# Kernel optimization log

Hardware: AMD Instinct MI355X
Metric: run time of the kernel (lower is better)

The kernel has to match this reference:

```python
import jax, jax.numpy as jnp
import numpy as np

B, C, L = 64, 21, 1024
D_MODEL, PATCH_LEN, STRIDE = 768, 16, 8


def setup_inputs() -> dict:
    key = jax.random.key(0)
    k1, k2, k3, k4 = jax.random.split(key, 4)
    x = jax.random.normal(k1, (B, C, L), dtype=jnp.float32)
    # Conv1d(patch_len -> d_model, k=3, circular, no bias), kaiming-ish scale
    conv_w = jax.random.normal(k2, (D_MODEL, PATCH_LEN, 3), dtype=jnp.float32) * (2.0 / (PATCH_LEN * 3)) ** 0.5
    w1 = jax.random.normal(k3, (D_MODEL, D_MODEL), dtype=jnp.float32) / np.float32(np.sqrt(D_MODEL))
    b1 = jnp.zeros((D_MODEL,), dtype=jnp.float32)
    w2 = jax.random.normal(k4, (D_MODEL, D_MODEL), dtype=jnp.float32) / np.float32(np.sqrt(D_MODEL))
    b2 = jnp.zeros((D_MODEL,), dtype=jnp.float32)
    return {"x": x, "conv_w": conv_w, "w1": w1, "b1": b1, "w2": w2, "b2": b2, "reverse": 0}


def _patchify(x):
    # ReplicationPad1d((0, stride)) then unfold(size=patch_len, step=stride)
    xp = jnp.pad(x, ((0, 0), (0, 0), (0, STRIDE)), mode="edge")  # (B,C,L+stride)
    P = (xp.shape[-1] - PATCH_LEN) // STRIDE + 1
    idx = jnp.arange(P)[:, None] * STRIDE + jnp.arange(PATCH_LEN)[None, :]  # (P, patch_len)
    patches = xp[:, :, idx]  # (B, C, P, patch_len)
    return patches.reshape(x.shape[0] * x.shape[1], P, PATCH_LEN)


def _token_embed(blocks, conv_w):
    # Conv1d over the patch axis, circular padding=1, no bias.
    h = blocks.transpose(0, 2, 1)  # (BN, patch_len, P)
    hp = jnp.concatenate([h[:, :, -1:], h, h[:, :, :1]], axis=-1)  # circular pad 1
    out = jax.lax.conv_general_dilated(
        hp, conv_w, window_strides=(1,), padding="VALID",
        dimension_numbers=("NCH", "OIH", "NCH"))  # (BN, d_model, P)
    return out.transpose(0, 2, 1)  # (BN, P, d_model)


def reference(x, conv_w, w1, b1, w2, b2, reverse):
    blocks = _patchify(x)  # (B*C, P, patch_len)
    # Note: in the original torch code, the reverse/cluster-flip branch writes
    # into a temporary produced by boolean indexing -> it is a value no-op.
    # reverse=0 here, so blocks pass through unchanged (faithful).
    emb = _token_embed(blocks, conv_w)  # (BN, P, d_model)
    pos = jnp.maximum(emb @ w1 + b1, 0.0) @ w2 + b2  # Linear-ReLU-Linear position MLP
    out = emb + pos  # dropout is identity at eval / p=0
    return out
```

## Files before the change

kernel.cpp:

```cpp
#include <hip/hip_runtime.h>
#include <hip/hip_bf16.h>

typedef __bf16 bf16x8 __attribute__((ext_vector_type(8)));
typedef float floatx4 __attribute__((ext_vector_type(4)));
typedef unsigned short ushort_t;
typedef ushort_t ushort8 __attribute__((ext_vector_type(8)));

#define KD 768

__global__ __launch_bounds__(256) void transpose_cvt_kernel(
    const float* __restrict__ src, __hip_bfloat16* __restrict__ dst) {
  __shared__ float tile[32][33];
  const int bx = blockIdx.x % 24;
  const int by = blockIdx.x / 24;
  const int tx = threadIdx.x & 31;
  const int ty = threadIdx.x >> 5;
#pragma unroll
  for (int i = 0; i < 32; i += 8)
    tile[ty + i][tx] = src[(size_t)(by * 32 + ty + i) * KD + bx * 32 + tx];
  __syncthreads();
#pragma unroll
  for (int i = 0; i < 32; i += 8)
    dst[(size_t)(bx * 32 + ty + i) * KD + by * 32 + tx] =
        __float2bfloat16(tile[tx][ty + i]);
}

__global__ __launch_bounds__(256) void w1c_kernel(
    const float* __restrict__ cw, const float* __restrict__ w1,
    __hip_bfloat16* __restrict__ w1ct) {
  __shared__ float wcrow[768];
  const int e = blockIdx.x;
  const int nb = blockIdx.y * 256 + threadIdx.x;
  const int i = e & 15, kk = e >> 4;
  for (int o = threadIdx.x; o < 768; o += 256)
    wcrow[o] = cw[(size_t)o * 48 + i * 3 + kk];
  __syncthreads();
  float acc = 0.f;
  for (int o = 0; o < 768; ++o)
    acc = fmaf(wcrow[o], w1[(size_t)o * KD + nb], acc);
  w1ct[(size_t)nb * 64 + e] = __float2bfloat16(acc);
  if (e == 0) {
#pragma unroll
    for (int ez = 48; ez < 64; ++ez)
      w1ct[(size_t)nb * 64 + ez] = __float2bfloat16(0.f);
  }
}

__global__ __launch_bounds__(128) void patchify_kernel(
    const float* __restrict__ x, __hip_bfloat16* __restrict__ P) {
  __shared__ float xs[1032];
  const int n = blockIdx.x;
  const int tid = threadIdx.x;
  const float* xr = x + (size_t)n * 1024;
  const float4* xr4 = (const float4*)xr;
  float4* xs4 = (float4*)xs;
  for (int j = tid; j < 256; j += 128) xs4[j] = xr4[j];
  if (tid < 8) xs[1024 + tid] = xr[1023];
  __syncthreads();
  const int p = tid;
  __hip_bfloat16 row[64];
#pragma unroll
  for (int kk = 0; kk < 3; ++kk) {
    const int q = (p + kk + 127) & 127;
#pragma unroll
    for (int i = 0; i < 16; ++i)
      row[kk * 16 + i] = __float2bfloat16(xs[q * 8 + i]);
  }
#pragma unroll
  for (int i = 48; i < 64; ++i) row[i] = __float2bfloat16(0.f);
  __hip_bfloat16* pr = P + ((size_t)n * 128 + p) * 64;
#pragma unroll
  for (int s = 0; s < 8; ++s)
    *(ushort8*)&pr[s * 8] = *(const ushort8*)&row[s * 8];
}

__device__ __forceinline__ void load_patch(const float* __restrict__ xr,
                                           int qw, float* b) {
  if (qw < 127) {
    const float4* p4 = (const float4*)(xr + qw * 8);
    float4 v0 = p4[0], v1 = p4[1], v2 = p4[2], v3 = p4[3];
    b[0] = v0.x; b[1] = v0.y; b[2] = v0.z; b[3] = v0.w;
    b[4] = v1.x; b[5] = v1.y; b[6] = v1.z; b[7] = v1.w;
    b[8] = v2.x; b[9] = v2.y; b[10] = v2.z; b[11] = v2.w;
    b[12] = v3.x; b[13] = v3.y; b[14] = v3.z; b[15] = v3.w;
  } else {
    float4 v0 = *(const float4*)(xr + 1016);
    float4 v1 = *(const float4*)(xr + 1020);
    b[0] = v0.x; b[1] = v0.y; b[2] = v0.z; b[3] = v0.w;
    b[4] = v1.x; b[5] = v1.y; b[6] = v1.z; b[7] = v1.w;
    float e = v1.w;
#pragma unroll
    for (int i = 8; i < 16; ++i) b[i] = e;
  }
}

__global__ __launch_bounds__(256) void conv_kernel(
    const float* __restrict__ x, const float* __restrict__ cw,
    __hip_bfloat16* __restrict__ emb, int nb) {
  const int lb = blockIdx.x;
  const int n = nb + lb;
  const float* xr = x + (size_t)n * 1024;
  const int o = blockIdx.y * 256 + threadIdx.x;

  float w[48];
  const float4* wp = (const float4*)(cw + (size_t)o * 48);
#pragma unroll
  for (int q = 0; q < 12; ++q) {
    float4 v = wp[q];
    w[q * 4 + 0] = v.x; w[q * 4 + 1] = v.y;
    w[q * 4 + 2] = v.z; w[q * 4 + 3] = v.w;
  }

  __hip_bfloat16* erow = emb + (size_t)lb * 128 * KD + o;
  float P0[16], P1[16], P2[16], P3[16];

  auto pair = [&](const float* Pa, const float* Pb, const float* Pc,
                  const float* Pd, int p) {
    float a0 = 0.f, a1 = 0.f;
#pragma unroll
    for (int i = 0; i < 16; ++i) {
      a0 += w[i * 3 + 0] * Pa[i];
      a0 += w[i * 3 + 1] * Pb[i];
      a0 += w[i * 3 + 2] * Pc[i];
      a1 += w[i * 3 + 0] * Pb[i];
      a1 += w[i * 3 + 1] * Pc[i];
      a1 += w[i * 3 + 2] * Pd[i];
    }
    erow[(size_t)p * KD] = __float2bfloat16(a0);
    erow[(size_t)(p + 1) * KD] = __float2bfloat16(a1);
  };

  load_patch(xr, 127, P0);
  load_patch(xr, 0, P1);
  for (int p = 0; p < 128; p += 4) {
    load_patch(xr, p + 1, P2);
    load_patch(xr, (p + 2) & 127, P3);
    pair(P0, P1, P2, P3, p);
    load_patch(xr, (p + 3) & 127, P0);
    load_patch(xr, (p + 4) & 127, P1);
    pair(P2, P3, P0, P1, p + 2);
  }
}

__global__ __launch_bounds__(512, 2) void pgemm_kernel(
    const __hip_bfloat16* __restrict__ P, const __hip_bfloat16* __restrict__ Bt,
    const float* __restrict__ bias, __hip_bfloat16* __restrict__ out) {
  __shared__ __align__(16) ushort_t As[256 * 64];
  __shared__ __align__(16) ushort_t Bs[256 * 64];
  const int tid = threadIdx.x;
  const int lane = tid & 63;
  const int w = __builtin_amdgcn_readfirstlane(tid >> 6);
  const int m0 = blockIdx.x * 256;
  const int n0 = blockIdx.y * 256;

  const int srow = tid >> 3;
  const int schunk = (tid & 7) ^ (srow & 7);
  const size_t ga = (size_t)(m0 + srow) * 64 + schunk * 8;
  const size_t gb = (size_t)(n0 + srow) * 64 + schunk * 8;
  typedef __attribute__((address_space(3))) void lv_t;
  typedef __attribute__((address_space(1))) const void gv_t;
  const int dw = w * 1024;
#pragma unroll
  for (int i = 0; i < 4; ++i)
    __builtin_amdgcn_global_load_lds(
        (gv_t*)(P + ga + (size_t)(i * 64) * 64),
        (lv_t*)((char*)&As[0] + i * 8192 + dw), 16, 0, 0);
#pragma unroll
  for (int i = 0; i < 4; ++i)
    __builtin_amdgcn_global_load_lds(
        (gv_t*)(Bt + gb + (size_t)(i * 64) * 64),
        (lv_t*)((char*)&Bs[0] + i * 8192 + dw), 16, 0, 0);
  asm volatile("s_waitcnt vmcnt(0)\n\ts_barrier" ::: "memory");

  const int rl = lane & 15;
  const int ql = lane >> 4;
  const int wm = (w >> 2) * 128;
  const int wn = (w & 3) * 64;
  const int so0 = (ql ^ (rl & 7)) * 8;
  const int ra = (wm + rl) * 64;
  const int rb = (wn + rl) * 64;

  floatx4 acc[8][4];
#pragma unroll
  for (int mi = 0; mi < 8; ++mi)
#pragma unroll
    for (int nj = 0; nj < 4; ++nj) acc[mi][nj] = (floatx4){0.f, 0.f, 0.f, 0.f};

#pragma unroll
  for (int ks = 0; ks < 2; ++ks) {
    const int so = so0 ^ (ks * 32);
    bf16x8 av[8], bv[4];
#pragma unroll
    for (int mi = 0; mi < 8; ++mi)
      av[mi] =
          __builtin_bit_cast(bf16x8, *(const ushort8*)&As[ra + mi * 1024 + so]);
#pragma unroll
    for (int nj = 0; nj < 4; ++nj)
      bv[nj] =
          __builtin_bit_cast(bf16x8, *(const ushort8*)&Bs[rb + nj * 1024 + so]);
#pragma unroll
    for (int mi = 0; mi < 8; ++mi)
#pragma unroll
      for (int nj = 0; nj < 4; ++nj)
        acc[mi][nj] = __builtin_amdgcn_mfma_f32_16x16x32_bf16(
            av[mi], bv[nj], acc[mi][nj], 0, 0, 0);
  }

#pragma unroll
  for (int nj = 0; nj < 4; ++nj) {
    const int cc = n0 + wn + nj * 16 + rl;
    const float bvs = bias[cc];
#pragma unroll
    for (int mi = 0; mi < 8; ++mi) {
      const int rbase = m0 + wm + mi * 16 + ql * 4;
#pragma unroll
      for (int p = 0; p < 4; ++p) {
        float v = acc[mi][nj][p] + bvs;
        v = v > 0.f ? v : 0.f;
        out[(size_t)(rbase + p) * KD + cc] = __float2bfloat16(v);
      }
    }
  }
}

template <int MODE>
__global__ __launch_bounds__(512, 2) void gemm_kernel(
    const __hip_bfloat16* __restrict__ A, const __hip_bfloat16* __restrict__ Bt,
    const float* __restrict__ bias, const __hip_bfloat16* __restrict__ emb,
    void* __restrict__ outp, int mt) {
  __shared__ __align__(16) ushort_t As[3 * 256 * 64];
  __shared__ __align__(16) ushort_t Bs[3 * 128 * 64];
  const int tid = threadIdx.x;
  const int lane = tid & 63;
  const int w = __builtin_amdgcn_readfirstlane(tid >> 6);

  const int total = mt * 6;
  const int q8 = total >> 3, r8 = total & 7;
  const int xcd = blockIdx.x & 7;
  const int j8 = blockIdx.x >> 3;
  const int wg =
      (xcd < r8 ? xcd * (q8 + 1) : r8 * (q8 + 1) + (xcd - r8) * q8) + j8;
  const int m0 = (wg / 6) * 256;
  const int n0 = (wg % 6) * 128;

  const int srow = tid >> 3;
  const int schunk = (tid & 7) ^ (srow & 7);
  const size_t ga = (size_t)(m0 + srow) * KD + schunk * 8;
  const size_t gb = (size_t)(n0 + srow) * KD + schunk * 8;
  typedef __attribute__((address_space(3))) void lv_t;
  typedef __attribute__((address_space(1))) const void gv_t;
  const int dw = w * 1024;

  auto stageA = [&](int t, int r3, int i) {
    __builtin_amdgcn_global_load_lds(
        (gv_t*)(A + ga + (size_t)(i * 64) * KD + t * 64),
        (lv_t*)((char*)&As[0] + r3 * 32768 + i * 8192 + dw), 16, 0, 0);
  };
  auto stageB = [&](int t, int r3, int j) {
    __builtin_amdgcn_global_load_lds(
        (gv_t*)(Bt + gb + (size_t)(j * 64) * KD + t * 64),
        (lv_t*)((char*)&Bs[0] + r3 * 16384 + j * 8192 + dw), 16, 0, 0);
  };

  const int rl = lane & 15;
  const int ql = lane >> 4;
  const int wm = (w >> 1) * 64;
  const int wn = (w & 1) * 64;
  const int so0 = (ql ^ (rl & 7)) * 8;
  const int ra = (wm + rl) * 64;
  const int rb = (wn + rl) * 64;

  floatx4 acc[4][4];
#pragma unroll
  for (int mi = 0; mi < 4; ++mi)
#pragma unroll
    for (int nj = 0; nj < 4; ++nj) acc[mi][nj] = (floatx4){0.f, 0.f, 0.f, 0.f};

#pragma unroll
  for (int i = 0; i < 4; ++i) stageA(0, 0, i);
#pragma unroll
  for (int j = 0; j < 2; ++j) stageB(0, 0, j);
#pragma unroll
  for (int i = 0; i < 4; ++i) stageA(1, 1, i);
#pragma unroll
  for (int j = 0; j < 2; ++j) stageB(1, 1, j);
  asm volatile("s_waitcnt vmcnt(6)\n\ts_barrier" ::: "memory");

  int rc = 0, rs = 2;
  for (int t = 0; t < 12; ++t) {
    const ushort_t* Ab = &As[rc * 16384];
    const ushort_t* Bb = &Bs[rc * 8192];
    bf16x8 av[4], bv[4];

#pragma unroll
    for (int mi = 0; mi < 4; ++mi)
      av[mi] =
          __builtin_bit_cast(bf16x8, *(const ushort8*)&Ab[ra + mi * 1024 + so0]);
#pragma unroll
    for (int nj = 0; nj < 4; ++nj)
      bv[nj] =
          __builtin_bit_cast(bf16x8, *(const ushort8*)&Bb[rb + nj * 1024 + so0]);
    if (t < 10) {
      stageA(t + 2, rs, 0);
      stageA(t + 2, rs, 1);
      stageA(t + 2, rs, 2);
    }
    asm volatile("s_barrier" ::: "memory");
    __builtin_amdgcn_s_setprio(1);
#pragma unroll
    for (int mi = 0; mi < 4; ++mi)
#pragma unroll
      for (int nj = 0; nj < 4; ++nj)
        acc[mi][nj] = __builtin_amdgcn_mfma_f32_16x16x32_bf16(
            av[mi], bv[nj], acc[mi][nj], 0, 0, 0);
    __builtin_amdgcn_s_setprio(0);
    asm volatile("s_barrier" ::: "memory");

    const int so1 = so0 ^ 32;
#pragma unroll
    for (int mi = 0; mi < 4; ++mi)
      av[mi] =
          __builtin_bit_cast(bf16x8, *(const ushort8*)&Ab[ra + mi * 1024 + so1]);
#pragma unroll
    for (int nj = 0; nj < 4; ++nj)
      bv[nj] =
          __builtin_bit_cast(bf16x8, *(const ushort8*)&Bb[rb + nj * 1024 + so1]);
    if (t < 10) {
      stageA(t + 2, rs, 3);
      stageB(t + 2, rs, 0);
      stageB(t + 2, rs, 1);
    }
    if (t < 10)
      asm volatile("s_waitcnt vmcnt(6)\n\ts_barrier" ::: "memory");
    else if (t == 10)
      asm volatile("s_waitcnt vmcnt(0)\n\ts_barrier" ::: "memory");
    else
      asm volatile("s_barrier" ::: "memory");
    __builtin_amdgcn_s_setprio(1);
#pragma unroll
    for (int mi = 0; mi < 4; ++mi)
#pragma unroll
      for (int nj = 0; nj < 4; ++nj)
        acc[mi][nj] = __builtin_amdgcn_mfma_f32_16x16x32_bf16(
            av[mi], bv[nj], acc[mi][nj], 0, 0, 0);
    __builtin_amdgcn_s_setprio(0);
    asm volatile("s_barrier" ::: "memory");

    rc = rc == 2 ? 0 : rc + 1;
    rs = rs == 2 ? 0 : rs + 1;
  }

#pragma unroll
  for (int nj = 0; nj < 4; ++nj) {
    const int cc = n0 + wn + nj * 16 + rl;
    const float bvs = bias[cc];
#pragma unroll
    for (int mi = 0; mi < 4; ++mi) {
      const int rbase = m0 + wm + mi * 16 + ql * 4;
#pragma unroll
      for (int p = 0; p < 4; ++p) {
        float v = acc[mi][nj][p] + bvs;
        if (MODE == 1) {
          v = v > 0.f ? v : 0.f;
          ((__hip_bfloat16*)outp)[(size_t)(rbase + p) * KD + cc] =
              __float2bfloat16(v);
        } else {
          v += __bfloat162float(emb[(size_t)(rbase + p) * KD + cc]);
          ((float*)outp)[(size_t)(rbase + p) * KD + cc] = v;
        }
      }
    }
  }
}

extern "C" void kernel_launch(void* const* d_in, const int* in_sizes, int n_in,
                              void* d_out, int out_size, void* d_ws,
                              size_t ws_size, hipStream_t stream) {
  const float* x = (const float*)d_in[0];
  const float* cw = (const float*)d_in[1];
  const float* w1 = (const float*)d_in[2];
  const float* b1 = (const float*)d_in[3];
  const float* w2 = (const float*)d_in[4];
  const float* b2 = (const float*)d_in[5];
  float* out = (float*)d_out;

  const size_t M_ALL = 1344 * 128;
  const size_t fixed = (size_t)KD * KD * 2 + (size_t)KD * 64 * 2 + M_ALL * 64 * 2;
  int NC = 4;
  while (NC < 32) {
    size_t cn_ = 1344 / NC;
    size_t need = fixed + 2 * cn_ * 128 * KD * 2;
    if (need <= ws_size) break;
    NC *= 2;
  }
  const int cn = 1344 / NC;
  const int mt = cn / 2;

  __hip_bfloat16* w2t = (__hip_bfloat16*)d_ws;
  __hip_bfloat16* w1ct = w2t + (size_t)KD * KD;
  __hip_bfloat16* Pm = w1ct + (size_t)KD * 64;
  __hip_bfloat16* embc = Pm + M_ALL * 64;
  __hip_bfloat16* hidc = embc + (size_t)cn * 128 * KD;

  transpose_cvt_kernel<<<576, 256, 0, stream>>>(w2, w2t);
  w1c_kernel<<<dim3(48, 3), 256, 0, stream>>>(cw, w1, w1ct);
  patchify_kernel<<<1344, 128, 0, stream>>>(x, Pm);

  for (int c = 0; c < NC; ++c) {
    const int nb = c * cn;
    conv_kernel<<<dim3(cn, 3), 256, 0, stream>>>(x, cw, embc, nb);
    pgemm_kernel<<<dim3(mt, 3), 512, 0, stream>>>(
        Pm + (size_t)nb * 128 * 64, w1ct, b1, hidc);
    gemm_kernel<2><<<dim3(mt * 6), 512, 0, stream>>>(
        hidc, w2t, b2, embc, (void*)(out + (size_t)nb * 128 * KD), mt);
  }
}
```

Measured before the change: 1.170 ms.

## Fold conv embedding into second GEMM as an extra K-tile

Drops the separate conv_kernel and the bf16 emb buffer. The residual emb term is computed inside the second GEMM as one extra 64-wide K step, multiplying the im2col patch matrix by a reordered conv weight matrix (wce). This removes a bandwidth-heavy conv pass, the emb write and its readback in the epilogue. The smaller workspace also allows fewer chunks. The cost is one more MFMA K-iteration per tile, a branch in the staging address computation, and the emb term now computed from bf16 inputs instead of fp32 x.

New measurement: 965.6 us. 1.21x faster.

```diff
diff --git a/kernel.cpp b/kernel.cpp
--- a/kernel.cpp
+++ b/kernel.cpp
@@ -46,6 +46,15 @@
   }
 }
 
+__global__ __launch_bounds__(64) void wce_kernel(
+    const float* __restrict__ cw, __hip_bfloat16* __restrict__ wce) {
+  const int o = blockIdx.x;
+  const int e = threadIdx.x;
+  float v = 0.f;
+  if (e < 48) v = cw[(size_t)o * 48 + (e & 15) * 3 + (e >> 4)];
+  wce[(size_t)o * 64 + e] = __float2bfloat16(v);
+}
+
 __global__ __launch_bounds__(128) void patchify_kernel(
     const float* __restrict__ x, __hip_bfloat16* __restrict__ P) {
   __shared__ float xs[1032];
@@ -74,74 +83,6 @@
     *(ushort8*)&pr[s * 8] = *(const ushort8*)&row[s * 8];
 }
 
-__device__ __forceinline__ void load_patch(const float* __restrict__ xr,
-                                           int qw, float* b) {
-  if (qw < 127) {
-    const float4* p4 = (const float4*)(xr + qw * 8);
-    float4 v0 = p4[0], v1 = p4[1], v2 = p4[2], v3 = p4[3];
-    b[0] = v0.x; b[1] = v0.y; b[2] = v0.z; b[3] = v0.w;
-    b[4] = v1.x; b[5] = v1.y; b[6] = v1.z; b[7] = v1.w;
-    b[8] = v2.x; b[9] = v2.y; b[10] = v2.z; b[11] = v2.w;
-    b[12] = v3.x; b[13] = v3.y; b[14] = v3.z; b[15] = v3.w;
-  } else {
-    float4 v0 = *(const float4*)(xr + 1016);
-    float4 v1 = *(const float4*)(xr + 1020);
-    b[0] = v0.x; b[1] = v0.y; b[2] = v0.z; b[3] = v0.w;
-    b[4] = v1.x; b[5] = v1.y; b[6] = v1.z; b[7] = v1.w;
-    float e = v1.w;
-#pragma unroll
-    for (int i = 8; i < 16; ++i) b[i] = e;
-  }
-}
-
-__global__ __launch_bounds__(256) void conv_kernel(
-    const float* __restrict__ x, const float* __restrict__ cw,
-    __hip_bfloat16* __restrict__ emb, int nb) {
-  const int lb = blockIdx.x;
-  const int n = nb + lb;
-  const float* xr = x + (size_t)n * 1024;
-  const int o = blockIdx.y * 256 + threadIdx.x;
-
-  float w[48];
-  const float4* wp = (const float4*)(cw + (size_t)o * 48);
-#pragma unroll
-  for (int q = 0; q < 12; ++q) {
-    float4 v = wp[q];
-    w[q * 4 + 0] = v.x; w[q * 4 + 1] = v.y;
-    w[q * 4 + 2] = v.z; w[q * 4 + 3] = v.w;
-  }
-
-  __hip_bfloat16* erow = emb + (size_t)lb * 128 * KD + o;
-  float P0[16], P1[16], P2[16], P3[16];
-
-  auto pair = [&](const float* Pa, const float* Pb, const float* Pc,
-                  const float* Pd, int p) {
-    float a0 = 0.f, a1 = 0.f;
-#pragma unroll
-    for (int i = 0; i < 16; ++i) {
-      a0 += w[i * 3 + 0] * Pa[i];
-      a0 += w[i * 3 + 1] * Pb[i];
-      a0 += w[i * 3 + 2] * Pc[i];
-      a1 += w[i * 3 + 0] * Pb[i];
-      a1 += w[i * 3 + 1] * Pc[i];
-      a1 += w[i * 3 + 2] * Pd[i];
-    }
-    erow[(size_t)p * KD] = __float2bfloat16(a0);
-    erow[(size_t)(p + 1) * KD] = __float2bfloat16(a1);
-  };
-
-  load_patch(xr, 127, P0);
-  load_patch(xr, 0, P1);
-  for (int p = 0; p < 128; p += 4) {
-    load_patch(xr, p + 1, P2);
-    load_patch(xr, (p + 2) & 127, P3);
-    pair(P0, P1, P2, P3, p);
-    load_patch(xr, (p + 3) & 127, P0);
-    load_patch(xr, (p + 4) & 127, P1);
-    pair(P2, P3, P0, P1, p + 2);
-  }
-}
-
 __global__ __launch_bounds__(512, 2) void pgemm_kernel(
     const __hip_bfloat16* __restrict__ P, const __hip_bfloat16* __restrict__ Bt,
     const float* __restrict__ bias, __hip_bfloat16* __restrict__ out) {
@@ -223,11 +164,12 @@
   }
 }
 
-template <int MODE>
-__global__ __launch_bounds__(512, 2) void gemm_kernel(
-    const __hip_bfloat16* __restrict__ A, const __hip_bfloat16* __restrict__ Bt,
-    const float* __restrict__ bias, const __hip_bfloat16* __restrict__ emb,
-    void* __restrict__ outp, int mt) {
+__global__ __launch_bounds__(512, 2) void gemm2f_kernel(
+    const __hip_bfloat16* __restrict__ A,
+    const __hip_bfloat16* __restrict__ Bt,
+    const __hip_bfloat16* __restrict__ P,
+    const __hip_bfloat16* __restrict__ WcE,
+    const float* __restrict__ bias, float* __restrict__ out, int mt) {
   __shared__ __align__(16) ushort_t As[3 * 256 * 64];
   __shared__ __align__(16) ushort_t Bs[3 * 128 * 64];
   const int tid = threadIdx.x;
@@ -247,19 +189,27 @@
   const int schunk = (tid & 7) ^ (srow & 7);
   const size_t ga = (size_t)(m0 + srow) * KD + schunk * 8;
   const size_t gb = (size_t)(n0 + srow) * KD + schunk * 8;
+  const size_t gap = (size_t)(m0 + srow) * 64 + schunk * 8;
+  const size_t gbp = (size_t)(n0 + srow) * 64 + schunk * 8;
   typedef __attribute__((address_space(3))) void lv_t;
   typedef __attribute__((address_space(1))) const void gv_t;
   const int dw = w * 1024;
 
   auto stageA = [&](int t, int r3, int i) {
+    const __hip_bfloat16* s =
+        (t == 12) ? (P + gap + (size_t)(i * 64) * 64)
+                  : (A + ga + (size_t)(i * 64) * KD + (size_t)t * 64);
     __builtin_amdgcn_global_load_lds(
-        (gv_t*)(A + ga + (size_t)(i * 64) * KD + t * 64),
-        (lv_t*)((char*)&As[0] + r3 * 32768 + i * 8192 + dw), 16, 0, 0);
+        (gv_t*)s, (lv_t*)((char*)&As[0] + r3 * 32768 + i * 8192 + dw), 16, 0,
+        0);
   };
   auto stageB = [&](int t, int r3, int j) {
+    const __hip_bfloat16* s =
+        (t == 12) ? (WcE + gbp + (size_t)(j * 64) * 64)
+                  : (Bt + gb + (size_t)(j * 64) * KD + (size_t)t * 64);
     __builtin_amdgcn_global_load_lds(
-        (gv_t*)(Bt + gb + (size_t)(j * 64) * KD + t * 64),
-        (lv_t*)((char*)&Bs[0] + r3 * 16384 + j * 8192 + dw), 16, 0, 0);
+        (gv_t*)s, (lv_t*)((char*)&Bs[0] + r3 * 16384 + j * 8192 + dw), 16, 0,
+        0);
   };
 
   const int rl = lane & 15;
@@ -287,7 +237,7 @@
   asm volatile("s_waitcnt vmcnt(6)\n\ts_barrier" ::: "memory");
 
   int rc = 0, rs = 2;
-  for (int t = 0; t < 12; ++t) {
+  for (int t = 0; t < 13; ++t) {
     const ushort_t* Ab = &As[rc * 16384];
     const ushort_t* Bb = &Bs[rc * 8192];
     bf16x8 av[4], bv[4];
@@ -300,7 +250,7 @@
     for (int nj = 0; nj < 4; ++nj)
       bv[nj] =
           __builtin_bit_cast(bf16x8, *(const ushort8*)&Bb[rb + nj * 1024 + so0]);
-    if (t < 10) {
+    if (t < 11) {
       stageA(t + 2, rs, 0);
       stageA(t + 2, rs, 1);
       stageA(t + 2, rs, 2);
@@ -325,14 +275,14 @@
     for (int nj = 0; nj < 4; ++nj)
       bv[nj] =
           __builtin_bit_cast(bf16x8, *(const ushort8*)&Bb[rb + nj * 1024 + so1]);
-    if (t < 10) {
+    if (t < 11) {
       stageA(t + 2, rs, 3);
       stageB(t + 2, rs, 0);
       stageB(t + 2, rs, 1);
     }
-    if (t < 10)
+    if (t < 11)
       asm volatile("s_waitcnt vmcnt(6)\n\ts_barrier" ::: "memory");
-    else if (t == 10)
+    else if (t == 11)
       asm volatile("s_waitcnt vmcnt(0)\n\ts_barrier" ::: "memory");
     else
       asm volatile("s_barrier" ::: "memory");
@@ -358,17 +308,8 @@
     for (int mi = 0; mi < 4; ++mi) {
       const int rbase = m0 + wm + mi * 16 + ql * 4;
 #pragma unroll
-      for (int p = 0; p < 4; ++p) {
-        float v = acc[mi][nj][p] + bvs;
-        if (MODE == 1) {
-          v = v > 0.f ? v : 0.f;
-          ((__hip_bfloat16*)outp)[(size_t)(rbase + p) * KD + cc] =
-              __float2bfloat16(v);
-        } else {
-          v += __bfloat162float(emb[(size_t)(rbase + p) * KD + cc]);
-          ((float*)outp)[(size_t)(rbase + p) * KD + cc] = v;
-        }
-      }
+      for (int p = 0; p < 4; ++p)
+        out[(size_t)(rbase + p) * KD + cc] = acc[mi][nj][p] + bvs;
     }
   }
 }
@@ -385,11 +326,12 @@
   float* out = (float*)d_out;
 
   const size_t M_ALL = 1344 * 128;
-  const size_t fixed = (size_t)KD * KD * 2 + (size_t)KD * 64 * 2 + M_ALL * 64 * 2;
-  int NC = 4;
+  const size_t fixed = (size_t)KD * KD * 2 + 2 * (size_t)KD * 64 * 2 +
+                       M_ALL * 64 * 2;
+  int NC = 2;
   while (NC < 32) {
     size_t cn_ = 1344 / NC;
-    size_t need = fixed + 2 * cn_ * 128 * KD * 2;
+    size_t need = fixed + cn_ * 128 * (size_t)KD * 2;
     if (need <= ws_size) break;
     NC *= 2;
   }
@@ -398,20 +340,21 @@
 
   __hip_bfloat16* w2t = (__hip_bfloat16*)d_ws;
   __hip_bfloat16* w1ct = w2t + (size_t)KD * KD;
-  __hip_bfloat16* Pm = w1ct + (size_t)KD * 64;
-  __hip_bfloat16* embc = Pm + M_ALL * 64;
-  __hip_bfloat16* hidc = embc + (size_t)cn * 128 * KD;
+  __hip_bfloat16* wce = w1ct + (size_t)KD * 64;
+  __hip_bfloat16* Pm = wce + (size_t)KD * 64;
+  __hip_bfloat16* hidc = Pm + M_ALL * 64;
 
   transpose_cvt_kernel<<<576, 256, 0, stream>>>(w2, w2t);
   w1c_kernel<<<dim3(48, 3), 256, 0, stream>>>(cw, w1, w1ct);
+  wce_kernel<<<768, 64, 0, stream>>>(cw, wce);
   patchify_kernel<<<1344, 128, 0, stream>>>(x, Pm);
 
   for (int c = 0; c < NC; ++c) {
     const int nb = c * cn;
-    conv_kernel<<<dim3(cn, 3), 256, 0, stream>>>(x, cw, embc, nb);
     pgemm_kernel<<<dim3(mt, 3), 512, 0, stream>>>(
         Pm + (size_t)nb * 128 * 64, w1ct, b1, hidc);
-    gemm_kernel<2><<<dim3(mt * 6), 512, 0, stream>>>(
-        hidc, w2t, b2, embc, (void*)(out + (size_t)nb * 128 * KD), mt);
-  }
-}
+    gemm2f_kernel<<<dim3(mt * 6), 512, 0, stream>>>(
+        hidc, w2t, Pm + (size_t)nb * 128 * 64, wce, b2,
+        out + (size_t)nb * 128 * KD, mt);
+  }
+}
```
